# Kernel tuning notes

Hardware: AMD Instinct MI355X
Metric: run time of the kernel (lower is better)

The kernel has to match this reference:

```python
import jax, jax.numpy as jnp
import numpy as np

EMBED_DIM = 1024
FFN_DIM = 4096
N_QUBITS = 16
BATCH, SEQ = 4, 2048


def setup_inputs() -> dict:
    key = jax.random.key(0)
    ks = jax.random.split(key, 6)
    s1 = 1.0 / np.sqrt(EMBED_DIM)
    s2 = 1.0 / np.sqrt(FFN_DIM)
    s3 = 1.0 / np.sqrt(N_QUBITS)
    return {
        "x": jax.random.normal(ks[0], (BATCH, SEQ, EMBED_DIM), jnp.float32),
        "W1": jax.random.normal(ks[1], (FFN_DIM, EMBED_DIM), jnp.float32) * s1,
        "Wq": jax.random.normal(ks[2], (N_QUBITS, FFN_DIM), jnp.float32) * s2,
        "theta": jax.random.normal(ks[3], (N_QUBITS,), jnp.float32),
        "W2": jax.random.normal(ks[4], (FFN_DIM, N_QUBITS), jnp.float32) * s3,
        "Wo": jax.random.normal(ks[5], (EMBED_DIM, FFN_DIM), jnp.float32) * s2,
    }


def reference(x, W1, Wq, theta, W2, Wo):
    # linear1: [b,s,e] @ [f,e]^T -> [b,s,f]
    h = jnp.einsum('bse,fe->bsf', x, W1)
    # to_qubits: [b,s,f] -> [b,s,q]
    q = jnp.einsum('bsf,qf->bsq', h, Wq)
    # Quantum circuit: RX(q_i) encoding then trainable RX(theta_i) per wire,
    # wires are unentangled product states -> <Z_i> = cos(q_i + theta_i).
    qm = jnp.cos(q + theta)
    # linear2 + relu
    h2 = jax.nn.relu(jnp.einsum('bsq,fq->bsf', qm, W2))
    # out_proj (dropout is identity in eval / p=0)
    return jnp.einsum('bsf,ef->bse', h2, Wo)
```

## Files before the change

### kernel.cpp

```cpp
#include <hip/hip_runtime.h>
#include <hip/hip_bf16.h>
#include <math.h>

typedef _Float16 f16;
typedef __attribute__((ext_vector_type(8))) _Float16 f16x8;
typedef __attribute__((ext_vector_type(4))) _Float16 f16x4;
typedef __attribute__((ext_vector_type(4))) float f32x4;

#define M_TOT 8192
#define E_DIM 1024
#define F_DIM 4096
#define NQ    16

#define BARRIER() asm volatile("s_barrier" ::: "memory")
#define WAITV(n)  asm volatile("s_waitcnt vmcnt(" #n ")" ::: "memory")
#define WAITLGKM() asm volatile("s_waitcnt lgkmcnt(0)" ::: "memory")

__device__ __forceinline__ f16x8 cvt8(float4 a, float4 b) {
    f16x8 o;
    o[0] = (f16)a.x; o[1] = (f16)a.y; o[2] = (f16)a.z; o[3] = (f16)a.w;
    o[4] = (f16)b.x; o[5] = (f16)b.y; o[6] = (f16)b.z; o[7] = (f16)b.w;
    return o;
}

__global__ __launch_bounds__(256) void prep_kernel(
    const float* __restrict__ W1, f16* __restrict__ W1t,
    const float* __restrict__ wo, f16* __restrict__ woh,
    const float* __restrict__ W2, f16* __restrict__ w2p)
{
    __shared__ float ls[64][68];
    const int b = blockIdx.x;
    if (b < 1024) {
        const int bf = b & 63;
        const int be = b >> 6;
        const int t  = threadIdx.x;
        const int r  = t >> 4;
        const int c4 = (t & 15) * 4;
        #pragma unroll
        for (int i = 0; i < 4; ++i) {
            int fr = r + i * 16;
            float4 v = *reinterpret_cast<const float4*>(W1 + (size_t)(bf * 64 + fr) * E_DIM + be * 64 + c4);
            ls[fr][c4] = v.x; ls[fr][c4 + 1] = v.y; ls[fr][c4 + 2] = v.z; ls[fr][c4 + 3] = v.w;
        }
        __syncthreads();
        const int er = t >> 2;
        const int fc = (t & 3) * 16;
        f16x8 o0, o1;
        #pragma unroll
        for (int j = 0; j < 8; ++j) { o0[j] = (f16)ls[fc + j][er]; o1[j] = (f16)ls[fc + 8 + j][er]; }
        f16* dst = W1t + (size_t)(be * 64 + er) * F_DIM + bf * 64 + fc;
        *reinterpret_cast<f16x8*>(dst)     = o0;
        *reinterpret_cast<f16x8*>(dst + 8) = o1;
    } else if (b < 3072) {
        size_t i = ((size_t)(b - 1024) * 256 + threadIdx.x) * 8;
        float4 v0 = *reinterpret_cast<const float4*>(wo + i);
        float4 v1 = *reinterpret_cast<const float4*>(wo + i + 4);
        *reinterpret_cast<f16x8*>(woh + i) = cvt8(v0, v1);
    } else {
        int t = (b - 3072) * 256 + threadIdx.x;
        size_t i = (size_t)t * 8;
        int col = (int)(i & 31);
        f16x8 o;
        if (col < NQ) {
            int row = (int)(i >> 5);
            float4 v0 = *reinterpret_cast<const float4*>(W2 + (size_t)row * NQ + col);
            float4 v1 = *reinterpret_cast<const float4*>(W2 + (size_t)row * NQ + col + 4);
            o = cvt8(v0, v1);
        } else {
            for (int k = 0; k < 8; ++k) o[k] = (f16)0.f;
        }
        *reinterpret_cast<f16x8*>(w2p + i) = o;
    }
}

__global__ __launch_bounds__(256) void tg_kernel(
    const float* __restrict__ Wq, const f16* __restrict__ W1t,
    float* __restrict__ pT)
{
    const int w = threadIdx.x >> 6, lane = threadIdx.x & 63;
    const int fr = lane & 15, fq = lane >> 4;
    const int kc = blockIdx.x & 15;
    const int et = blockIdx.x >> 4;
    const int e0 = et * 128 + w * 32;
    const int kbase = kc * 256;

    f32x4 acc[2] = {};
    #pragma unroll
    for (int s = 0; s < 8; ++s) {
        int k = kbase + s * 32 + fq * 8;
        float4 a0 = *reinterpret_cast<const float4*>(Wq + (size_t)fr * F_DIM + k);
        float4 a1 = *reinterpret_cast<const float4*>(Wq + (size_t)fr * F_DIM + k + 4);
        f16x8 af = cvt8(a0, a1);
        #pragma unroll
        for (int n = 0; n < 2; ++n) {
            f16x8 bf = *reinterpret_cast<const f16x8*>(W1t + (size_t)(e0 + n * 16 + fr) * F_DIM + k);
            acc[n] = __builtin_amdgcn_mfma_f32_16x16x32_f16(af, bf, acc[n], 0, 0, 0);
        }
    }
    #pragma unroll
    for (int n = 0; n < 2; ++n)
        #pragma unroll
        for (int j = 0; j < 4; ++j)
            pT[(size_t)kc * (16 * E_DIM) + (size_t)(fq * 4 + j) * E_DIM + e0 + n * 16 + fr] = acc[n][j];
}

__global__ __launch_bounds__(256) void treduce_kernel(
    const float* __restrict__ pT, f16* __restrict__ Th)
{
    int idx = blockIdx.x * 256 + threadIdx.x;
    float s = 0.f;
    #pragma unroll
    for (int kc = 0; kc < 16; ++kc) s += pT[(size_t)kc * (16 * E_DIM) + idx];
    Th[idx] = (f16)s;
}

__global__ __launch_bounds__(512) void qx2_kernel(
    const float* __restrict__ x, const f16* __restrict__ Th,
    const float* __restrict__ theta, f16* __restrict__ qmp)
{
    __shared__ __align__(16) f16 ths[16 * 1024];
    __shared__ float pql[2048];
    const int tid = threadIdx.x, w = tid >> 6, lane = tid & 63;
    const int fr = lane & 15, fq = lane >> 4;
    const int m0 = blockIdx.x * 64;

    #pragma unroll
    for (int i = 0; i < 4; ++i) {
        int tau = i * 512 + tid;
        int q   = tau >> 7;
        int kb  = tau & 127;
        f16x8 v = *reinterpret_cast<const f16x8*>(Th + (size_t)q * E_DIM + kb * 8);
        int boff = (q * 2048 + kb * 16) ^ ((q & 7) << 4);
        *reinterpret_cast<f16x8*>((char*)ths + boff) = v;
    }
    __syncthreads();

    const int kc = w >> 2;
    const int rg = w & 3;
    const float* xa = x + (size_t)(m0 + rg * 16 + fr) * E_DIM + kc * 512;
    f32x4 acc = {};
    #pragma unroll
    for (int s = 0; s < 16; ++s) {
        int ko = s * 32 + fq * 8;
        float4 a0 = *reinterpret_cast<const float4*>(xa + ko);
        float4 a1 = *reinterpret_cast<const float4*>(xa + ko + 4);
        f16x8 af = cvt8(a0, a1);
        int boff = (fr * 2048 + (kc * 512 + ko) * 2) ^ ((fr & 7) << 4);
        f16x8 bf = *reinterpret_cast<const f16x8*>((char*)ths + boff);
        acc = __builtin_amdgcn_mfma_f32_16x16x32_f16(af, bf, acc, 0, 0, 0);
    }
    #pragma unroll
    for (int j = 0; j < 4; ++j)
        pql[(kc * 64 + rg * 16 + fq * 4 + j) * 16 + fr] = acc[j];
    __syncthreads();

    #pragma unroll
    for (int e = 0; e < 2; ++e) {
        int idx = e * 512 + tid;
        int row = idx >> 4, q = idx & 15;
        float s = pql[idx] + pql[1024 + idx];
        float v = cosf(s + theta[q]);
        qmp[(size_t)(m0 + row) * 32 + q]      = (f16)v;
        qmp[(size_t)(m0 + row) * 32 + 16 + q] = (f16)0.f;
    }
}

__device__ __forceinline__ void gload_lds16(const f16* g, f16* l) {
    __builtin_amdgcn_global_load_lds(
        (const __attribute__((address_space(1))) void*)(g),
        (__attribute__((address_space(3))) void*)(l), 16, 0, 0);
}

__global__ __launch_bounds__(512, 2)
void gemm4f(const f16* __restrict__ qmp, const f16* __restrict__ w2p,
            const f16* __restrict__ Wo, f16* __restrict__ P0, f16* __restrict__ P1)
{
    extern __shared__ __align__(16) f16 smem[];
    const int tid  = threadIdx.x;
    const int w    = tid >> 6;
    const int lane = tid & 63;

    const int nwg = gridDim.x;
    const int bid = blockIdx.x;
    const int cpx = nwg >> 3;
    int swz = (bid & 7) * cpx + (bid >> 3);
    const int per = nwg >> 1;
    const int split = swz / per;
    const int r = swz % per;
    const int by = r >> 2, bx = r & 3;
    const int m0 = by * 256, n0 = bx * 256;

    const int wr = w >> 2, wc = w & 3;
    const int fr = lane & 15, fq = lane >> 4;
    const int K = 2048;

    const f16* Bb  = Wo + (size_t)split * K;
    const f16* w2g = w2p + (size_t)split * K * 32;
    f16* Pout = split ? P1 : P0;

    const int r0w = w * 32 + fr;
    f16x8 qreg0 = *reinterpret_cast<const f16x8*>(qmp + (size_t)(m0 + r0w) * 32 + fq * 8);
    f16x8 qreg1 = *reinterpret_cast<const f16x8*>(qmp + (size_t)(m0 + r0w + 16) * 32 + fq * 8);

    const int rl   = w * 8 + (lane >> 3);
    const int scol = (((lane & 7) ^ (rl & 7)) * 8);
    const f16* gB = Bb + (size_t)(n0 + rl) * F_DIM + scol;
    f16* lB = smem + 16384 + w * 512;

#define SB(b,h,j,kt) gload_lds16(gB + (size_t)((h)*128 + (j)*64) * F_DIM + (kt), lB + (b)*32768 + (h)*8192 + (j)*4096)
#define SBH(b,h,kt) do { SB(b,h,0,kt); SB(b,h,1,kt); } while(0)

    f16x8 w2a[4], w2b[4];
#define LOADW2(R, kt) do { _Pragma("unroll") \
    for (int ft = 0; ft < 4; ++ft) \
        R[ft] = *reinterpret_cast<const f16x8*>(w2g + (size_t)((kt) + ft*16 + fr) * 32 + fq * 8); } while(0)

#define PRODUCE(bdst, W2R) do {                                                   \
    f32x4 z_ = {0.f, 0.f, 0.f, 0.f};                                              \
    _Pragma("unroll") for (int ft = 0; ft < 4; ++ft) {                            \
        f32x4 c0_ = __builtin_amdgcn_mfma_f32_16x16x32_f16(W2R[ft], qreg0, z_, 0, 0, 0); \
        f32x4 c1_ = __builtin_amdgcn_mfma_f32_16x16x32_f16(W2R[ft], qreg1, z_, 0, 0, 0); \
        f16x4 h0_, h1_;                                                           \
        _Pragma("unroll") for (int jj = 0; jj < 4; ++jj) {                        \
            h0_[jj] = (f16)fmaxf(c0_[jj], 0.f); h1_[jj] = (f16)fmaxf(c1_[jj], 0.f); } \
        const int sl_ = (2 * ft + (fq >> 1)) ^ (fr & 7);                          \
        *reinterpret_cast<f16x4*>(smem + (bdst)*32768 + (r0w)*64      + sl_*8 + ((fq & 1) << 2)) = h0_; \
        *reinterpret_cast<f16x4*>(smem + (bdst)*32768 + (r0w+16)*64   + sl_*8 + ((fq & 1) << 2)) = h1_; \
    } } while(0)

    const int xm  = fr & 7;
    const int so0 = ((0 + fq) ^ xm) * 8;
    const int so1 = ((4 + fq) ^ xm) * 8;
    const int aro = (wr * 128 + fr) * 64;
    const int bro = (wc * 64  + fr) * 64;

#define AF(b,m,ks) (*reinterpret_cast<const f16x8*>(smem + (b)*32768 + aro + (m)*1024 + so##ks))
#define BF(b,n,ks) (*reinterpret_cast<const f16x8*>(smem + (b)*32768 + 16384 + bro + (n)*1024 + so##ks))

    f32x4 acc[8][4] = {};
    f16x8 bf[4][2];

#define PHASE(b, p, STAGES, W4) do {                                              \
    f16x8 a00 = AF(b, 2*(p),   0), a01 = AF(b, 2*(p),   1);                       \
    f16x8 a10 = AF(b, 2*(p)+1, 0), a11 = AF(b, 2*(p)+1, 1);                       \
    if ((p) == 0) { _Pragma("unroll")                                             \
        for (int n = 0; n < 4; ++n) { bf[n][0] = BF(b,n,0); bf[n][1] = BF(b,n,1); } } \
    STAGES;                                                                       \
    BARRIER();                                                                    \
    __builtin_amdgcn_s_setprio(1);                                                \
    _Pragma("unroll") for (int n = 0; n < 4; ++n) {                               \
        acc[2*(p)  ][n] = __builtin_amdgcn_mfma_f32_16x16x32_f16(a00, bf[n][0], acc[2*(p)  ][n], 0,0,0); \
        acc[2*(p)+1][n] = __builtin_amdgcn_mfma_f32_16x16x32_f16(a10, bf[n][0], acc[2*(p)+1][n], 0,0,0); } \
    _Pragma("unroll") for (int n = 0; n < 4; ++n) {                               \
        acc[2*(p)  ][n] = __builtin_amdgcn_mfma_f32_16x16x32_f16(a01, bf[n][1], acc[2*(p)  ][n], 0,0,0); \
        acc[2*(p)+1][n] = __builtin_amdgcn_mfma_f32_16x16x32_f16(a11, bf[n][1], acc[2*(p)+1][n], 0,0,0); } \
    __builtin_amdgcn_s_setprio(0);                                                \
    if (W4) { WAITV(8); WAITLGKM(); }                                             \
    BARRIER(); } while(0)

    const int NT = K >> 6;
    const int NI = NT >> 1;

    LOADW2(w2b, 0);
    LOADW2(w2a, 64);
    SBH(0,0,0);  SBH(0,1,0);
    SBH(1,0,64); SBH(1,1,64);
    WAITV(0);
    BARRIER();
    PRODUCE(0, w2b);
    WAITLGKM();
    BARRIER();

    for (int i = 0; i < NI; ++i) {
        int t2 = 2*i+2; if (t2 > NT-1) t2 = NT-1;
        int t3 = 2*i+3; if (t3 > NT-1) t3 = NT-1;
        const int k2 = t2 << 6, k3 = t3 << 6;
        PHASE(0, 0, PRODUCE(1, w2a),            0);
        PHASE(0, 1, LOADW2(w2b, k2); SBH(0,0,k2), 0);
        PHASE(0, 2, SBH(0,1,k2),                0);
        PHASE(0, 3, ,                           1);
        PHASE(1, 0, PRODUCE(0, w2b),            0);
        PHASE(1, 1, LOADW2(w2a, k3); SBH(1,0,k3), 0);
        PHASE(1, 2, SBH(1,1,k3),                0);
        PHASE(1, 3, ,                           1);
    }
    WAITV(0);

    #pragma unroll
    for (int m = 0; m < 8; ++m) {
        #pragma unroll
        for (int n = 0; n < 4; ++n) {
            #pragma unroll
            for (int j = 0; j < 4; ++j) {
                int row = m0 + wr * 128 + m * 16 + fq * 4 + j;
                int col = n0 + wc * 64  + n * 16 + fr;
                Pout[(size_t)row * E_DIM + col] = (f16)acc[m][n][j];
            }
        }
    }
#undef SB
#undef SBH
#undef LOADW2
#undef PRODUCE
#undef AF
#undef BF
#undef PHASE
}

__global__ __launch_bounds__(256) void out_reduce2_kernel(
    float* __restrict__ out, const f16* __restrict__ p0, const f16* __restrict__ p1)
{
    size_t i = ((size_t)blockIdx.x * 256 + threadIdx.x) * 8;
    f16x8 a = *reinterpret_cast<const f16x8*>(p0 + i);
    f16x8 b = *reinterpret_cast<const f16x8*>(p1 + i);
    float4 v0, v1;
    v0.x = (float)a[0] + (float)b[0]; v0.y = (float)a[1] + (float)b[1];
    v0.z = (float)a[2] + (float)b[2]; v0.w = (float)a[3] + (float)b[3];
    v1.x = (float)a[4] + (float)b[4]; v1.y = (float)a[5] + (float)b[5];
    v1.z = (float)a[6] + (float)b[6]; v1.w = (float)a[7] + (float)b[7];
    *reinterpret_cast<float4*>(out + i)     = v0;
    *reinterpret_cast<float4*>(out + i + 4) = v1;
}

extern "C" void kernel_launch(void* const* d_in, const int* in_sizes, int n_in,
                              void* d_out, int out_size, void* d_ws, size_t ws_size,
                              hipStream_t stream) {
    const float* x  = (const float*)d_in[0];
    const float* W1 = (const float*)d_in[1];
    const float* Wq = (const float*)d_in[2];
    const float* th = (const float*)d_in[3];
    const float* W2 = (const float*)d_in[4];
    const float* Wo = (const float*)d_in[5];
    float* out = (float*)d_out;

    char* base = (char*)d_ws;
    float* pT  = (float*)base;
    f16*   Th  = (f16*)(base + (1 << 20));
    f16*   w1t = (f16*)(base + 16777216);
    f16*   woh = w1t + (size_t)E_DIM * F_DIM;
    f16*   w2p = woh + (size_t)E_DIM * F_DIM;
    f16*   qmp = w2p + (size_t)F_DIM * 32;
    f16*   p0  = qmp + (size_t)M_TOT * 32;
    f16*   p1  = p0  + (size_t)M_TOT * E_DIM;

    static bool attr_done = false;
    if (!attr_done) {
        hipFuncSetAttribute((const void*)&gemm4f,
                            hipFuncAttributeMaxDynamicSharedMemorySize, 131072);
        attr_done = true;
    }

    prep_kernel<<<3136, 256, 0, stream>>>(W1, w1t, Wo, woh, W2, w2p);
    tg_kernel<<<128, 256, 0, stream>>>(Wq, w1t, pT);
    treduce_kernel<<<64, 256, 0, stream>>>(pT, Th);
    qx2_kernel<<<128, 512, 0, stream>>>(x, Th, th, qmp);
    gemm4f<<<256, 512, 131072, stream>>>(qmp, w2p, woh, p0, p1);
    out_reduce2_kernel<<<4096, 256, 0, stream>>>(out, p0, p1);
}
```

Before: 114.0 us.

## Compute Wq·W1 product directly from fp32 W1, drop W1 transpose pass

Removes the W1 transpose-and-convert step from the prep kernel and replaces the MFMA-based Wq·W1 kernel with a scalar fp32 kernel that reads W1 directly in its native layout, coalesced along the embedding dimension. This eliminates writing and re-reading an 8 MB fp16 transposed copy of W1. In exchange, the partial-sum buffer grows to 64 chunks, the reduce kernel reads four times as much, and the product uses scalar FMAs instead of matrix cores.

```diff
diff --git a/kernel.cpp b/kernel.cpp
--- a/kernel.cpp
+++ b/kernel.cpp
@@ -24,40 +24,17 @@
 }
 
 __global__ __launch_bounds__(256) void prep_kernel(
-    const float* __restrict__ W1, f16* __restrict__ W1t,
     const float* __restrict__ wo, f16* __restrict__ woh,
     const float* __restrict__ W2, f16* __restrict__ w2p)
 {
-    __shared__ float ls[64][68];
     const int b = blockIdx.x;
-    if (b < 1024) {
-        const int bf = b & 63;
-        const int be = b >> 6;
-        const int t  = threadIdx.x;
-        const int r  = t >> 4;
-        const int c4 = (t & 15) * 4;
-        #pragma unroll
-        for (int i = 0; i < 4; ++i) {
-            int fr = r + i * 16;
-            float4 v = *reinterpret_cast<const float4*>(W1 + (size_t)(bf * 64 + fr) * E_DIM + be * 64 + c4);
-            ls[fr][c4] = v.x; ls[fr][c4 + 1] = v.y; ls[fr][c4 + 2] = v.z; ls[fr][c4 + 3] = v.w;
-        }
-        __syncthreads();
-        const int er = t >> 2;
-        const int fc = (t & 3) * 16;
-        f16x8 o0, o1;
-        #pragma unroll
-        for (int j = 0; j < 8; ++j) { o0[j] = (f16)ls[fc + j][er]; o1[j] = (f16)ls[fc + 8 + j][er]; }
-        f16* dst = W1t + (size_t)(be * 64 + er) * F_DIM + bf * 64 + fc;
-        *reinterpret_cast<f16x8*>(dst)     = o0;
-        *reinterpret_cast<f16x8*>(dst + 8) = o1;
-    } else if (b < 3072) {
-        size_t i = ((size_t)(b - 1024) * 256 + threadIdx.x) * 8;
+    if (b < 2048) {
+        size_t i = ((size_t)b * 256 + threadIdx.x) * 8;
         float4 v0 = *reinterpret_cast<const float4*>(wo + i);
         float4 v1 = *reinterpret_cast<const float4*>(wo + i + 4);
         *reinterpret_cast<f16x8*>(woh + i) = cvt8(v0, v1);
     } else {
-        int t = (b - 3072) * 256 + threadIdx.x;
+        int t = (b - 2048) * 256 + threadIdx.x;
         size_t i = (size_t)t * 8;
         int col = (int)(i & 31);
         f16x8 o;
@@ -73,44 +50,35 @@
     }
 }
 
-__global__ __launch_bounds__(256) void tg_kernel(
-    const float* __restrict__ Wq, const f16* __restrict__ W1t,
-    float* __restrict__ pT)
-{
-    const int w = threadIdx.x >> 6, lane = threadIdx.x & 63;
-    const int fr = lane & 15, fq = lane >> 4;
-    const int kc = blockIdx.x & 15;
-    const int et = blockIdx.x >> 4;
-    const int e0 = et * 128 + w * 32;
-    const int kbase = kc * 256;
-
-    f32x4 acc[2] = {};
-    #pragma unroll
-    for (int s = 0; s < 8; ++s) {
-        int k = kbase + s * 32 + fq * 8;
-        float4 a0 = *reinterpret_cast<const float4*>(Wq + (size_t)fr * F_DIM + k);
-        float4 a1 = *reinterpret_cast<const float4*>(Wq + (size_t)fr * F_DIM + k + 4);
-        f16x8 af = cvt8(a0, a1);
+__global__ __launch_bounds__(256) void tgd_kernel(
+    const float* __restrict__ Wq, const float* __restrict__ W1,
+    float* __restrict__ pT2)
+{
+    const int kc = blockIdx.x >> 2;
+    const int eb = blockIdx.x & 3;
+    const int e  = eb * 256 + threadIdx.x;
+    const int f0 = kc * 64;
+    float acc[16] = {};
+    #pragma unroll 4
+    for (int fi = 0; fi < 64; ++fi) {
+        int f = f0 + fi;
+        float w1v = W1[(size_t)f * E_DIM + e];
         #pragma unroll
-        for (int n = 0; n < 2; ++n) {
-            f16x8 bf = *reinterpret_cast<const f16x8*>(W1t + (size_t)(e0 + n * 16 + fr) * F_DIM + k);
-            acc[n] = __builtin_amdgcn_mfma_f32_16x16x32_f16(af, bf, acc[n], 0, 0, 0);
-        }
-    }
-    #pragma unroll
-    for (int n = 0; n < 2; ++n)
-        #pragma unroll
-        for (int j = 0; j < 4; ++j)
-            pT[(size_t)kc * (16 * E_DIM) + (size_t)(fq * 4 + j) * E_DIM + e0 + n * 16 + fr] = acc[n][j];
+        for (int q = 0; q < 16; ++q)
+            acc[q] += Wq[(size_t)q * F_DIM + f] * w1v;
+    }
+    #pragma unroll
+    for (int q = 0; q < 16; ++q)
+        pT2[(size_t)kc * (16 * E_DIM) + (size_t)q * E_DIM + e] = acc[q];
 }
 
 __global__ __launch_bounds__(256) void treduce_kernel(
-    const float* __restrict__ pT, f16* __restrict__ Th)
+    const float* __restrict__ pT2, f16* __restrict__ Th)
 {
     int idx = blockIdx.x * 256 + threadIdx.x;
     float s = 0.f;
     #pragma unroll
-    for (int kc = 0; kc < 16; ++kc) s += pT[(size_t)kc * (16 * E_DIM) + idx];
+    for (int kc = 0; kc < 64; ++kc) s += pT2[(size_t)kc * (16 * E_DIM) + idx];
     Th[idx] = (f16)s;
 }
 
@@ -334,8 +302,8 @@
     float* out = (float*)d_out;
 
     char* base = (char*)d_ws;
-    float* pT  = (float*)base;
-    f16*   Th  = (f16*)(base + (1 << 20));
+    float* pT2 = (float*)base;
+    f16*   Th  = (f16*)(base + (4 << 20));
     f16*   w1t = (f16*)(base + 16777216);
     f16*   woh = w1t + (size_t)E_DIM * F_DIM;
     f16*   w2p = woh + (size_t)E_DIM * F_DIM;
@@ -350,9 +318,9 @@
         attr_done = true;
     }
 
-    prep_kernel<<<3136, 256, 0, stream>>>(W1, w1t, Wo, woh, W2, w2p);
-    tg_kernel<<<128, 256, 0, stream>>>(Wq, w1t, pT);
-    treduce_kernel<<<64, 256, 0, stream>>>(pT, Th);
+    prep_kernel<<<2112, 256, 0, stream>>>(Wo, woh, W2, w2p);
+    tgd_kernel<<<256, 256, 0, stream>>>(Wq, W1, pT2);
+    treduce_kernel<<<64, 256, 0, stream>>>(pT2, Th);
     qx2_kernel<<<128, 512, 0, stream>>>(x, Th, th, qmp);
     gemm4f<<<256, 512, 131072, stream>>>(qmp, w2p, woh, p0, p1);
     out_reduce2_kernel<<<4096, 256, 0, stream>>>(out, p0, p1);
```

Measured after the change: 129.7 us. 13.8% more time.
